# Optimization experiments

Measured on AMD Instinct MI355X. Metric: run time of the kernel, lower is better.

Reference implementation:

```python
import jax, jax.numpy as jnp
import numpy as np

H = 96
W = 96
FX = 96.0
FY = 96.0
NEAR = 0.3
EPS = 1e-8


def q2r(quat):
    # quat: [N,4] (w,x,y,z) -> [N,3,3]
    q = quat / (jnp.linalg.norm(quat, axis=-1, keepdims=True) + 1e-12)
    w, x, y, z = q[:, 0], q[:, 1], q[:, 2], q[:, 3]
    R = jnp.stack([
        1 - 2 * (y * y + z * z), 2 * (x * y - w * z), 2 * (x * z + w * y),
        2 * (x * y + w * z), 1 - 2 * (x * x + z * z), 2 * (y * z - w * x),
        2 * (x * z - w * y), 2 * (y * z + w * x), 1 - 2 * (x * x + y * y),
    ], axis=-1).reshape(-1, 3, 3)
    return R


def setup_inputs() -> dict:
    key = jax.random.key(0)
    ks = jax.random.split(key, 8)
    N = 4096
    pos_xy = jax.random.uniform(ks[0], (N, 2), minval=-2.0, maxval=2.0, dtype=jnp.float32)
    pos_z = jax.random.uniform(ks[1], (N, 1), minval=2.0, maxval=6.0, dtype=jnp.float32)
    pos = jnp.concatenate([pos_xy, pos_z], axis=-1)
    rgb = jax.random.normal(ks[2], (N, 3), dtype=jnp.float32)
    opa = jax.random.normal(ks[3], (N,), dtype=jnp.float32)
    quat = jax.random.normal(ks[4], (N, 4), dtype=jnp.float32)
    scale = jax.random.uniform(ks[5], (N, 3), dtype=jnp.float32) * 0.05 + 0.005
    rot = jnp.eye(3, dtype=jnp.float32)
    tran = jnp.zeros(3, dtype=jnp.float32)
    return {"pos": pos, "rgb": rgb, "opa": opa, "quat": quat, "scale": scale, "rot": rot, "tran": tran}


def reference(pos, rgb, opa, quat, scale, rot, tran):
    # ---- project: world -> camera -> image space ----
    cam = pos @ rot.T + tran[None, :]              # [N,3]
    x, y, z = cam[:, 0], cam[:, 1], cam[:, 2]
    r = jnp.linalg.norm(cam, axis=-1)              # depth = ray length (camera_to_image)
    mean2d = jnp.stack([x / z, y / z], axis=-1)    # [N,2]

    # jacobian of (x/z, y/z, |p|) wrt camera-space point, [N,3,3]
    zeros = jnp.zeros_like(z)
    J = jnp.stack([
        1.0 / z, zeros, -x / (z * z),
        zeros, 1.0 / z, -y / (z * z),
        x / r, y / r, z / r,
    ], axis=-1).reshape(-1, 3, 3)

    # ---- 3D covariance: R S S^T R^T ----
    R = q2r(quat)                                   # [N,3,3]
    s = jnp.abs(scale) + 1e-4                       # [N,3]
    RS = R * s[:, None, :]                          # R @ diag(s)
    cov3d = jnp.einsum('nij,nkj->nik', RS, RS)      # [N,3,3]

    # ---- 2D covariance: (J W) cov3d (J W)^T, upper-left 2x2 ----
    JW = jnp.einsum('nij,jk->nik', J, rot)          # [N,3,3]
    cov2d = jnp.einsum('nij,njk,nlk->nil', JW, cov3d, JW)[:, :2, :2]  # [N,2,2]

    a = cov2d[:, 0, 0] + EPS
    d = cov2d[:, 1, 1] + EPS
    b = 0.5 * (cov2d[:, 0, 1] + cov2d[:, 1, 0])
    det = a * d - b * b
    inv_a = d / det
    inv_b = -b / det
    inv_d = a / det

    rgb_act = jax.nn.sigmoid(rgb)                   # [N,3]
    opa_act = jax.nn.sigmoid(opa)                   # [N]

    # ---- per-pixel gaussian evaluation in normalized image space ----
    u = (jnp.arange(W, dtype=jnp.float32) + 0.5 - W / 2) / FX   # [W]
    v = (jnp.arange(H, dtype=jnp.float32) + 0.5 - H / 2) / FY   # [H]
    pu = jnp.tile(u, H)                                          # [P]
    pv = jnp.repeat(v, W)                                        # [P]

    dx = pu[None, :] - mean2d[:, 0:1]               # [N,P]
    dy = pv[None, :] - mean2d[:, 1:2]               # [N,P]
    power = -0.5 * (inv_a[:, None] * dx * dx + 2.0 * inv_b[:, None] * dx * dy + inv_d[:, None] * dy * dy)
    alpha = opa_act[:, None] * jnp.exp(power)       # [N,P]
    alpha = jnp.clip(alpha, 0.0, 0.99)
    valid = (z > NEAR).astype(alpha.dtype)[:, None]
    alpha = alpha * valid

    # ---- depth-sorted alpha compositing ----
    order = jnp.argsort(r)                          # near -> far
    alpha_s = alpha[order]                          # [N,P]
    rgb_s = rgb_act[order]                          # [N,3]

    log_1m = jnp.log1p(-alpha_s)                    # [N,P]
    cum = jnp.cumsum(log_1m, axis=0)
    logT = jnp.concatenate([jnp.zeros((1, alpha_s.shape[1]), alpha_s.dtype), cum[:-1]], axis=0)
    w = jnp.exp(logT) * alpha_s                     # [N,P] blending weights
    img = jnp.einsum('np,nc->pc', w, rgb_s)         # [P,3]
    return img.reshape(H, W, 3)
```

## Files before the change

### kernel.cpp

```cpp
#include <hip/hip_runtime.h>
#include <math.h>

#define N_G   4096
#define IMW   96
#define TILE  6
#define TILES_X 16
#define NTILE (TILES_X*TILES_X)
#define NTHR  1024
#define NW    (NTHR/64)
#define NST   (N_G/NTHR)
#define NPX   (TILE*TILE)
#define NSEG  16
#define BCAP  1536
#define CAP   512
#define FXI   (1.0f/96.0f)
#define NEARP 0.3f
#define EPSV  1e-8f
#define LOG2E 1.4426950408889634f
#define LN2   0.6931471805599453f
#define CULL_K 26.0f

typedef unsigned long long ull;
typedef __attribute__((ext_vector_type(2))) unsigned long long ull2;

__global__ __launch_bounds__(NTHR, 1) void splat_k(
    const float* __restrict__ pos, const float* __restrict__ rgb,
    const float* __restrict__ opa, const float* __restrict__ quat,
    const float* __restrict__ scale, const float* __restrict__ rot,
    const float* __restrict__ tran, float* __restrict__ out)
{
    __shared__ unsigned int bl[BCAP];
    __shared__ __align__(16) ull skey[CAP+4];
    __shared__ float4 g0[CAP], g1[CAP];
    __shared__ float  g2[CAP];
    __shared__ float4 pix[NSEG*NPX];
    __shared__ int wsA[NST][NW];
    __shared__ int wsB[NW];
    __shared__ int psum[2][CAP];
    __shared__ float4 stash[N_G];
    __shared__ float  rrs[N_G];

    const int t = threadIdx.x;
    const int tile = blockIdx.x;
    const int tx = tile % TILES_X, ty = tile / TILES_X;
    const float u0 = ((float)(tx*TILE) + 0.5f - 48.0f) * FXI;
    const float u1 = u0 + (TILE-1) * FXI;
    const float v0 = ((float)(ty*TILE) + 0.5f - 48.0f) * FXI;
    const float v1 = v0 + (TILE-1) * FXI;
    const int wid = t >> 6, lane = t & 63;

    float R00=rot[0],R01=rot[1],R02=rot[2];
    float R10=rot[3],R11=rot[4],R12=rot[5];
    float R20=rot[6],R21=rot[7],R22=rot[8];
    float t0=tran[0], t1=tran[1], t2=tran[2];

    float pp0[NST], pp1[NST], pp2[NST], po[NST], ps0[NST], ps1[NST], ps2[NST];
    #pragma unroll
    for (int st = 0; st < NST; st++) {
        int gi = st*NTHR + t;
        pp0[st]=pos[gi*3+0]; pp1[st]=pos[gi*3+1]; pp2[st]=pos[gi*3+2];
        po[st]=opa[gi];
        ps0[st]=scale[gi*3+0]; ps1[st]=scale[gi*3+1]; ps2[st]=scale[gi*3+2];
    }

    int bcnt = 0;
    #pragma unroll
    for (int st = 0; st < NST; st++) {
        int gi = st*NTHR + t;
        float x = R00*pp0[st] + R01*pp1[st] + R02*pp2[st] + t0;
        float y = R10*pp0[st] + R11*pp1[st] + R12*pp2[st] + t1;
        float z = R20*pp0[st] + R21*pp1[st] + R22*pp2[st] + t2;
        float rr = sqrtf(x*x + y*y + z*z);
        float invz = 1.0f/z;
        float mu = x*invz, mv = y*invz;

        float sig_o = 1.0f/(1.0f+__expf(-po[st]));
        float opa_eff = (z > NEARP) ? sig_o : 0.0f;
        stash[gi] = make_float4(mu, mv, z, opa_eff);
        rrs[gi] = rr;

        float inz2 = invz*invz;
        float fn = 2.0f*inz2 + (x*x + y*y)*inz2*inz2;
        float smax = fmaxf(fmaxf(fabsf(ps0[st]), fabsf(ps1[st])), fabsf(ps2[st])) + 1e-4f;
        float lmax = fn*smax*smax + EPSV;
        float amp = CULL_K + 1.0f + log2f(opa_eff);
        float r2b = amp * lmax * (2.0f*LN2) * 1.02f;

        float cu = fminf(fmaxf(mu, u0), u1);
        float cv = fminf(fmaxf(mv, v0), v1);
        float ddx = mu - cu, ddy = mv - cv;
        bool flag = (amp > 0.0f) && (ddx*ddx + ddy*ddy <= r2b);

        ull m = __ballot(flag);
        if (lane == 0) wsA[st][wid] = __popcll(m);
        __syncthreads();
        int base = bcnt, tot = 0;
        #pragma unroll
        for (int w = 0; w < NW; w++) { int c = wsA[st][w]; if (w < wid) base += c; tot += c; }
        if (flag) {
            int p = base + __popcll(m & ((1ull << lane) - 1ull));
            if (p < BCAP) bl[p] = (unsigned int)gi;
        }
        bcnt += tot;
    }
    if (bcnt > BCAP) bcnt = BCAP;
    __syncthreads();

    int cnt = 0;
    for (int s0i = 0; s0i < bcnt; s0i += NTHR) {
        int s = s0i + t;
        bool flag = false;
        float4 o0, o1; float ocb = 0.0f, rr = 0.0f;
        if (s < bcnt) {
            int gi = bl[s];
            float4 sg = stash[gi];
            rr = rrs[gi];
            float mu = sg.x, mv = sg.y, z = sg.z, opa_eff = sg.w;
            float invz = 1.0f/z;

            float J02 = -mu*invz, J12 = -mv*invz;
            float JW00 = invz*R00 + J02*R20;
            float JW01 = invz*R01 + J02*R21;
            float JW02 = invz*R02 + J02*R22;
            float JW10 = invz*R10 + J12*R20;
            float JW11 = invz*R11 + J12*R21;
            float JW12 = invz*R12 + J12*R22;

            const float4 qv = ((const float4*)quat)[gi];
            float qw=qv.x, qx=qv.y, qy=qv.z, qz=qv.w;
            float qn = sqrtf(qw*qw+qx*qx+qy*qy+qz*qz) + 1e-12f;
            float qi = 1.0f/qn;
            qw*=qi; qx*=qi; qy*=qi; qz*=qi;
            float Q00=1.f-2.f*(qy*qy+qz*qz), Q01=2.f*(qx*qy-qw*qz), Q02=2.f*(qx*qz+qw*qy);
            float Q10=2.f*(qx*qy+qw*qz), Q11=1.f-2.f*(qx*qx+qz*qz), Q12=2.f*(qy*qz-qw*qx);
            float Q20=2.f*(qx*qz-qw*qy), Q21=2.f*(qy*qz+qw*qx), Q22=1.f-2.f*(qx*qx+qy*qy);

            float sa=fabsf(scale[gi*3+0])+1e-4f;
            float sb=fabsf(scale[gi*3+1])+1e-4f;
            float sc=fabsf(scale[gi*3+2])+1e-4f;
            float A00=Q00*sa,A01=Q01*sb,A02=Q02*sc;
            float A10=Q10*sa,A11=Q11*sb,A12=Q12*sc;
            float A20=Q20*sa,A21=Q21*sb,A22=Q22*sc;
            float C00=A00*A00+A01*A01+A02*A02;
            float C01=A00*A10+A01*A11+A02*A12;
            float C02=A00*A20+A01*A21+A02*A22;
            float C11=A10*A10+A11*A11+A12*A12;
            float C12=A10*A20+A11*A21+A12*A22;
            float C22=A20*A20+A21*A21+A22*A22;
            float M00=JW00*C00+JW01*C01+JW02*C02;
            float M01=JW00*C01+JW01*C11+JW02*C12;
            float M02=JW00*C02+JW01*C12+JW02*C22;
            float M10=JW10*C00+JW11*C01+JW12*C02;
            float M11=JW10*C01+JW11*C11+JW12*C12;
            float M12=JW10*C02+JW11*C12+JW12*C22;
            float a  = M00*JW00+M01*JW01+M02*JW02 + EPSV;
            float d  = M10*JW10+M11*JW11+M12*JW12 + EPSV;
            float bb = 0.5f*((M00*JW10+M01*JW11+M02*JW12)+(M10*JW00+M11*JW01+M12*JW02));
            float invdet = 1.0f/(a*d - bb*bb);
            float iaP = -0.5f*d*invdet*LOG2E;
            float ibP =  bb*invdet*LOG2E;
            float idP = -0.5f*a*invdet*LOG2E;

            float q00 = -iaP, q01 = -0.5f*ibP, q11 = -idP;
            float df = q00 - q11;
            float lam = 0.5f*((q00 + q11) - sqrtf(df*df + 4.0f*q01*q01));
            lam = fmaxf(lam, 1e-20f);
            float r2 = (CULL_K + log2f(opa_eff)) / lam;

            float cu = fminf(fmaxf(mu, u0), u1);
            float cv = fminf(fmaxf(mv, v0), v1);
            float ddx = mu - cu, ddy = mv - cv;
            flag = (ddx*ddx + ddy*ddy) <= r2;

            if (flag) {
                float c0 = 1.0f/(1.0f+__expf(-rgb[gi*3+0]));
                float c1 = 1.0f/(1.0f+__expf(-rgb[gi*3+1]));
                float c2 = 1.0f/(1.0f+__expf(-rgb[gi*3+2]));
                o0 = make_float4(mu, mv, iaP, ibP);
                o1 = make_float4(idP, opa_eff, c0, c1);
                ocb = c2;
            }
        }
        ull m = __ballot(flag);
        if (lane == 0) wsB[wid] = __popcll(m);
        __syncthreads();
        int base = cnt, tot = 0;
        #pragma unroll
        for (int w = 0; w < NW; w++) { int c = wsB[w]; if (w < wid) base += c; tot += c; }
        if (flag) {
            int p = base + __popcll(m & ((1ull << lane) - 1ull));
            if (p < CAP) {
                g0[p] = o0; g1[p] = o1; g2[p] = ocb;
                skey[p] = ((ull)__float_as_uint(rr) << 32) | (unsigned int)p;
            }
        }
        cnt += tot;
        __syncthreads();
    }
    if (cnt > CAP) cnt = CAP;

    int cnt2 = cnt + (cnt & 1);
    if (t == 0 && (cnt & 1)) skey[cnt] = ~0ull;
    __syncthreads();
    int h = ((cnt2 >> 1) + 1) & ~1;
    if (h > cnt2) h = cnt2;
    const int g = t >> 9, e = t & 511;
    ull v = 0;
    if (e < cnt) {
        v = skey[e];
        const ull2* sk2 = (const ull2*)skey;
        int wA2 = g ? (h >> 1) : 0;
        int wB2 = g ? (cnt2 >> 1) : (h >> 1);
        int c = 0;
        for (int w = wA2; w < wB2; w++) {
            ull2 p = sk2[w];
            c += (p.x < v) ? 1 : 0;
            c += (p.y < v) ? 1 : 0;
        }
        psum[g][e] = c;
    }
    __syncthreads();
    if (t < cnt) {
        int r = psum[0][t] + psum[1][t];
        skey[r] = v;
    }
    __syncthreads();

    if (t < NSEG*NPX) {
        const int seg = t / NPX, pid = t % NPX;
        const int px = tx*TILE + (pid % TILE);
        const int py = ty*TILE + (pid / TILE);
        const float pu = ((float)px + 0.5f - 48.0f) * FXI;
        const float pv = ((float)py + 0.5f - 48.0f) * FXI;

        const int per = (cnt + NSEG - 1) / NSEG;
        const int sA = min(seg * per, cnt);
        const int sB = min(sA + per, cnt);

        float T = 1.0f, cr = 0.0f, cg = 0.0f, cb = 0.0f;
        for (int s = sA; s < sB; s++) {
            int slot = (int)(skey[s] & 0xffffffffu);
            float4 a0 = g0[slot];
            float4 a1 = g1[slot];
            float a2 = g2[slot];
            float dx = pu - a0.x;
            float dy = pv - a0.y;
            float pw = dx*(a0.z*dx + a0.w*dy) + a1.x*dy*dy;
            float al = fminf(a1.y * __builtin_amdgcn_exp2f(pw), 0.99f);
            float w = T * al;
            cr += w * a1.z;
            cg += w * a1.w;
            cb += w * a2;
            T *= (1.0f - al);
        }
        pix[t] = make_float4(cr, cg, cb, T);
    }
    __syncthreads();

    if (t < NPX) {
        float orr = 0.0f, og = 0.0f, ob = 0.0f, T2 = 1.0f;
        #pragma unroll
        for (int s = 0; s < NSEG; s++) {
            float4 P = pix[s*NPX + t];
            orr += T2 * P.x;
            og  += T2 * P.y;
            ob  += T2 * P.z;
            T2  *= P.w;
        }
        int px = tx*TILE + (t % TILE);
        int py = ty*TILE + (t / TILE);
        int pixel = py * IMW + px;
        out[pixel*3+0] = orr;
        out[pixel*3+1] = og;
        out[pixel*3+2] = ob;
    }
}

extern "C" void kernel_launch(void* const* d_in, const int* in_sizes, int n_in,
                              void* d_out, int out_size, void* d_ws, size_t ws_size,
                              hipStream_t stream) {
    const float* pos   = (const float*)d_in[0];
    const float* rgb   = (const float*)d_in[1];
    const float* opa   = (const float*)d_in[2];
    const float* quat  = (const float*)d_in[3];
    const float* scale = (const float*)d_in[4];
    const float* rot   = (const float*)d_in[5];
    const float* tran  = (const float*)d_in[6];
    float* out = (float*)d_out;

    splat_k<<<NTILE, NTHR, 0, stream>>>(pos, rgb, opa, quat, scale, rot, tran, out);
}
```

Before: 15.76 us.

## Replace block-wide prefix scans with wave atomics and drop shared stash arrays

```diff
diff --git a/kernel.cpp b/kernel.cpp
--- a/kernel.cpp
+++ b/kernel.cpp
@@ -11,7 +11,7 @@
 #define NST   (N_G/NTHR)
 #define NPX   (TILE*TILE)
 #define NSEG  16
-#define BCAP  1536
+#define BCAP  2048
 #define CAP   512
 #define FXI   (1.0f/96.0f)
 #define NEARP 0.3f
@@ -30,15 +30,13 @@
     const float* __restrict__ tran, float* __restrict__ out)
 {
     __shared__ unsigned int bl[BCAP];
-    __shared__ __align__(16) ull skey[CAP+4];
+    __shared__ __align__(16) ull skey[CAP+2];
+    __shared__ int sslot[CAP];
     __shared__ float4 g0[CAP], g1[CAP];
     __shared__ float  g2[CAP];
     __shared__ float4 pix[NSEG*NPX];
-    __shared__ int wsA[NST][NW];
-    __shared__ int wsB[NW];
     __shared__ int psum[2][CAP];
-    __shared__ float4 stash[N_G];
-    __shared__ float  rrs[N_G];
+    __shared__ int bcnt_sh, cnt_sh;
 
     const int t = threadIdx.x;
     const int tile = blockIdx.x;
@@ -47,7 +45,9 @@
     const float u1 = u0 + (TILE-1) * FXI;
     const float v0 = ((float)(ty*TILE) + 0.5f - 48.0f) * FXI;
     const float v1 = v0 + (TILE-1) * FXI;
-    const int wid = t >> 6, lane = t & 63;
+    const int lane = t & 63;
+
+    if (t == 0) { bcnt_sh = 0; cnt_sh = 0; }
 
     float R00=rot[0],R01=rot[1],R02=rot[2];
     float R10=rot[3],R11=rot[4],R12=rot[5];
@@ -62,63 +62,58 @@
         po[st]=opa[gi];
         ps0[st]=scale[gi*3+0]; ps1[st]=scale[gi*3+1]; ps2[st]=scale[gi*3+2];
     }
-
-    int bcnt = 0;
+    __syncthreads();
+
     #pragma unroll
     for (int st = 0; st < NST; st++) {
         int gi = st*NTHR + t;
         float x = R00*pp0[st] + R01*pp1[st] + R02*pp2[st] + t0;
         float y = R10*pp0[st] + R11*pp1[st] + R12*pp2[st] + t1;
         float z = R20*pp0[st] + R21*pp1[st] + R22*pp2[st] + t2;
-        float rr = sqrtf(x*x + y*y + z*z);
         float invz = 1.0f/z;
         float mu = x*invz, mv = y*invz;
-
-        float sig_o = 1.0f/(1.0f+__expf(-po[st]));
-        float opa_eff = (z > NEARP) ? sig_o : 0.0f;
-        stash[gi] = make_float4(mu, mv, z, opa_eff);
-        rrs[gi] = rr;
 
         float inz2 = invz*invz;
         float fn = 2.0f*inz2 + (x*x + y*y)*inz2*inz2;
         float smax = fmaxf(fmaxf(fabsf(ps0[st]), fabsf(ps1[st])), fabsf(ps2[st])) + 1e-4f;
         float lmax = fn*smax*smax + EPSV;
-        float amp = CULL_K + 1.0f + log2f(opa_eff);
+        float amp = CULL_K + 1.0f + fminf(0.0f, po[st]*LOG2E);
         float r2b = amp * lmax * (2.0f*LN2) * 1.02f;
 
         float cu = fminf(fmaxf(mu, u0), u1);
         float cv = fminf(fmaxf(mv, v0), v1);
         float ddx = mu - cu, ddy = mv - cv;
-        bool flag = (amp > 0.0f) && (ddx*ddx + ddy*ddy <= r2b);
+        bool flag = (z > NEARP) && (amp > 0.0f) && (ddx*ddx + ddy*ddy <= r2b);
 
         ull m = __ballot(flag);
-        if (lane == 0) wsA[st][wid] = __popcll(m);
-        __syncthreads();
-        int base = bcnt, tot = 0;
-        #pragma unroll
-        for (int w = 0; w < NW; w++) { int c = wsA[st][w]; if (w < wid) base += c; tot += c; }
+        int nm = __popcll(m);
+        int base = 0;
+        if (lane == 0 && nm) base = atomicAdd(&bcnt_sh, nm);
+        base = __shfl(base, 0);
         if (flag) {
             int p = base + __popcll(m & ((1ull << lane) - 1ull));
             if (p < BCAP) bl[p] = (unsigned int)gi;
         }
-        bcnt += tot;
-    }
-    if (bcnt > BCAP) bcnt = BCAP;
-    __syncthreads();
-
-    int cnt = 0;
+    }
+    __syncthreads();
+    int bcnt = bcnt_sh; if (bcnt > BCAP) bcnt = BCAP;
+
     for (int s0i = 0; s0i < bcnt; s0i += NTHR) {
         int s = s0i + t;
         bool flag = false;
         float4 o0, o1; float ocb = 0.0f, rr = 0.0f;
+        unsigned int gi = 0;
         if (s < bcnt) {
-            int gi = bl[s];
-            float4 sg = stash[gi];
-            rr = rrs[gi];
-            float mu = sg.x, mv = sg.y, z = sg.z, opa_eff = sg.w;
+            gi = bl[s];
+            float p0=pos[gi*3+0], p1=pos[gi*3+1], p2=pos[gi*3+2];
+            float x = R00*p0 + R01*p1 + R02*p2 + t0;
+            float y = R10*p0 + R11*p1 + R12*p2 + t1;
+            float z = R20*p0 + R21*p1 + R22*p2 + t2;
+            rr = sqrtf(x*x + y*y + z*z);
             float invz = 1.0f/z;
-
-            float J02 = -mu*invz, J12 = -mv*invz;
+            float mu = x*invz, mv = y*invz;
+
+            float J02 = -x*invz*invz, J12 = -y*invz*invz;
             float JW00 = invz*R00 + J02*R20;
             float JW01 = invz*R01 + J02*R21;
             float JW02 = invz*R02 + J02*R22;
@@ -126,8 +121,7 @@
             float JW11 = invz*R11 + J12*R21;
             float JW12 = invz*R12 + J12*R22;
 
-            const float4 qv = ((const float4*)quat)[gi];
-            float qw=qv.x, qx=qv.y, qy=qv.z, qz=qv.w;
+            float qw=quat[gi*4+0], qx=quat[gi*4+1], qy=quat[gi*4+2], qz=quat[gi*4+3];
             float qn = sqrtf(qw*qw+qx*qx+qy*qy+qz*qz) + 1e-12f;
             float qi = 1.0f/qn;
             qw*=qi; qx*=qi; qy*=qi; qz*=qi;
@@ -161,6 +155,9 @@
             float ibP =  bb*invdet*LOG2E;
             float idP = -0.5f*a*invdet*LOG2E;
 
+            float sig_o = 1.0f/(1.0f+__expf(-opa[gi]));
+            float opa_eff = (z > NEARP) ? sig_o : 0.0f;
+
             float q00 = -iaP, q01 = -0.5f*ibP, q11 = -idP;
             float df = q00 - q11;
             float lam = 0.5f*((q00 + q11) - sqrtf(df*df + 4.0f*q01*q01));
@@ -182,26 +179,24 @@
             }
         }
         ull m = __ballot(flag);
-        if (lane == 0) wsB[wid] = __popcll(m);
-        __syncthreads();
-        int base = cnt, tot = 0;
-        #pragma unroll
-        for (int w = 0; w < NW; w++) { int c = wsB[w]; if (w < wid) base += c; tot += c; }
+        int nm = __popcll(m);
+        int base = 0;
+        if (lane == 0 && nm) base = atomicAdd(&cnt_sh, nm);
+        base = __shfl(base, 0);
         if (flag) {
             int p = base + __popcll(m & ((1ull << lane) - 1ull));
             if (p < CAP) {
                 g0[p] = o0; g1[p] = o1; g2[p] = ocb;
-                skey[p] = ((ull)__float_as_uint(rr) << 32) | (unsigned int)p;
+                skey[p] = ((ull)__float_as_uint(rr) << 32) | gi;
             }
         }
-        cnt += tot;
-        __syncthreads();
-    }
-    if (cnt > CAP) cnt = CAP;
-
+    }
+    __syncthreads();
+    int cnt = cnt_sh; if (cnt > CAP) cnt = CAP;
+
+    if (t == 0 && (cnt & 1)) skey[cnt] = ~0ull;
+    __syncthreads();
     int cnt2 = cnt + (cnt & 1);
-    if (t == 0 && (cnt & 1)) skey[cnt] = ~0ull;
-    __syncthreads();
     int h = ((cnt2 >> 1) + 1) & ~1;
     if (h > cnt2) h = cnt2;
     const int g = t >> 9, e = t & 511;
@@ -209,10 +204,10 @@
     if (e < cnt) {
         v = skey[e];
         const ull2* sk2 = (const ull2*)skey;
-        int wA2 = g ? (h >> 1) : 0;
-        int wB2 = g ? (cnt2 >> 1) : (h >> 1);
+        int wA = g ? (h >> 1) : 0;
+        int wB = g ? (cnt2 >> 1) : (h >> 1);
         int c = 0;
-        for (int w = wA2; w < wB2; w++) {
+        for (int w = wA; w < wB; w++) {
             ull2 p = sk2[w];
             c += (p.x < v) ? 1 : 0;
             c += (p.y < v) ? 1 : 0;
@@ -222,7 +217,8 @@
     __syncthreads();
     if (t < cnt) {
         int r = psum[0][t] + psum[1][t];
-        skey[r] = v;
+        skey[r]  = v;
+        sslot[r] = t;
     }
     __syncthreads();
 
@@ -239,10 +235,10 @@
 
         float T = 1.0f, cr = 0.0f, cg = 0.0f, cb = 0.0f;
         for (int s = sA; s < sB; s++) {
-            int slot = (int)(skey[s] & 0xffffffffu);
+            int slot = sslot[s];
             float4 a0 = g0[slot];
             float4 a1 = g1[slot];
-            float a2 = g2[slot];
+            float  a2 = g2[slot];
             float dx = pu - a0.x;
             float dy = pv - a0.y;
             float pw = dx*(a0.z*dx + a0.w*dy) + a1.x*dy*dy;
```

New measurement: 14.59 us. 7.5% less time.
